# Performance work log

Measured on AMD Instinct MI355X. Metric: run time of the kernel, lower is better.

## Reference

```python
import jax, jax.numpy as jnp
import numpy as np

IN_F = 4096
OUT_F = 12288
GROUPSIZE = 128
BATCH = 8
N_GROUPS = IN_F // GROUPSIZE  # 32


def setup_inputs() -> dict:
    key = jax.random.key(0)
    k1, k2, k3, k4 = jax.random.split(key, 4)
    x = jax.random.normal(k1, (BATCH, IN_F), dtype=jnp.float32)
    # int4 codes in [0, 16)
    qweight = jax.random.randint(k2, (OUT_F, IN_F), 0, 16, dtype=jnp.int32)
    # per-group scales (positive, small) and zeros, layout [in//groupsize, out]
    scales = jax.random.uniform(k3, (N_GROUPS, OUT_F), dtype=jnp.float32) * 0.02 + 1e-3
    zeros = jax.random.normal(k4, (N_GROUPS, OUT_F), dtype=jnp.float32) * 0.1
    return {"x": x, "qweight": qweight, "scales": scales, "zeros": zeros}


def reference(x, qweight, scales, zeros):
    # Dequantize int4 weights: w = (q - 8) * scale + zero, per group of 128 along K.
    # qweight: [OUT_F, IN_F] -> [OUT_F, N_GROUPS, GROUPSIZE]
    q = qweight.reshape(OUT_F, N_GROUPS, GROUPSIZE).astype(jnp.float32)
    s = scales.T[:, :, None]  # [OUT_F, N_GROUPS, 1]
    z = zeros.T[:, :, None]   # [OUT_F, N_GROUPS, 1]
    w = ((q - 8.0) * s + z).reshape(OUT_F, IN_F)  # dequantized fp weight
    # Linear: y = x @ w.T  -> [BATCH, OUT_F]
    return jnp.einsum('bk,nk->bn', x, w)
```

## Files before the change

### kernel.cpp

```cpp
#include <hip/hip_runtime.h>

#define IN_F 4096
#define OUT_F 12288
#define BATCH 8
#define NGROUPS 32

#define CHUNK 256
#define NCHUNKS (IN_F / CHUNK)
#define ROWS_PER_WAVE 6
#define ROWS_PER_BLOCK 48
#define NBLOCKS (OUT_F / ROWS_PER_BLOCK)
#define THREADS 512

__global__ __launch_bounds__(THREADS, 2)
void w4a32_gemv(const float* __restrict__ x,
                const int* __restrict__ qw,
                const float* __restrict__ scales,
                const float* __restrict__ zeros,
                float* __restrict__ out)
{
    __shared__ float xs[BATCH][IN_F];
    __shared__ float szs[NGROUPS * ROWS_PER_BLOCK];
    __shared__ float szc[NGROUPS * ROWS_PER_BLOCK];

    const int tid   = threadIdx.x;
    const int wave  = tid >> 6;
    const int lane  = tid & 63;
    const int rowb  = blockIdx.x * ROWS_PER_BLOCK;
    const int wrow  = wave * ROWS_PER_WAVE;
    const int klane = lane << 2;

    const int* qbase = qw + (size_t)(rowb + wrow) * IN_F + klane;

    int4 qA[ROWS_PER_WAVE], qB[ROWS_PER_WAVE];
#pragma unroll
    for (int r = 0; r < ROWS_PER_WAVE; ++r)
        qA[r] = *reinterpret_cast<const int4*>(qbase + r * IN_F);

#pragma unroll
    for (int j = 0; j < 16; ++j) {
        const int idx = tid + j * THREADS;
        const int b   = idx >> 10;
        const int kk  = (idx & 1023) << 2;
        *reinterpret_cast<float4*>(&xs[b][kk]) =
            *reinterpret_cast<const float4*>(&x[b * IN_F + kk]);
    }
#pragma unroll
    for (int j = 0; j < 4; ++j) {
        const int idx = tid + j * THREADS;
        const int g   = idx >> 6;
        const int r   = idx & 63;
        if (r < ROWS_PER_BLOCK) {
            const float s = scales[g * OUT_F + rowb + r];
            const float z = zeros [g * OUT_F + rowb + r];
            szs[g * ROWS_PER_BLOCK + r] = s;
            szc[g * ROWS_PER_BLOCK + r] = __builtin_fmaf(s, -8.f, z);
        }
    }
    __syncthreads();

    float acc[ROWS_PER_WAVE][BATCH];
#pragma unroll
    for (int r = 0; r < ROWS_PER_WAVE; ++r)
#pragma unroll
        for (int b = 0; b < BATCH; ++b) acc[r][b] = 0.f;

    auto consume = [&](const int4 (&q)[ROWS_PER_WAVE], const int k0c) {
        const int g = (k0c >> 7) + (lane >> 5);
        float4 xr[BATCH];
#pragma unroll
        for (int b = 0; b < BATCH; ++b)
            xr[b] = *reinterpret_cast<const float4*>(&xs[b][k0c + klane]);
#pragma unroll
        for (int r = 0; r < ROWS_PER_WAVE; ++r) {
            const float s  = szs[g * ROWS_PER_BLOCK + wrow + r];
            const float cc = szc[g * ROWS_PER_BLOCK + wrow + r];
            const float w0 = __builtin_fmaf((float)q[r].x, s, cc);
            const float w1 = __builtin_fmaf((float)q[r].y, s, cc);
            const float w2 = __builtin_fmaf((float)q[r].z, s, cc);
            const float w3 = __builtin_fmaf((float)q[r].w, s, cc);
#pragma unroll
            for (int b = 0; b < BATCH; ++b) {
                float a = acc[r][b];
                a = __builtin_fmaf(w0, xr[b].x, a);
                a = __builtin_fmaf(w1, xr[b].y, a);
                a = __builtin_fmaf(w2, xr[b].z, a);
                a = __builtin_fmaf(w3, xr[b].w, a);
                acc[r][b] = a;
            }
        }
    };

    for (int c = 0; c < NCHUNKS; c += 2) {
        const int k0 = c * CHUNK;
#pragma unroll
        for (int r = 0; r < ROWS_PER_WAVE; ++r)
            qB[r] = *reinterpret_cast<const int4*>(qbase + r * IN_F + k0 + CHUNK);

        consume(qA, k0);

        if (c + 2 < NCHUNKS) {
#pragma unroll
            for (int r = 0; r < ROWS_PER_WAVE; ++r)
                qA[r] = *reinterpret_cast<const int4*>(qbase + r * IN_F + k0 + 2 * CHUNK);
        }

        consume(qB, k0 + CHUNK);
    }

#pragma unroll
    for (int r = 0; r < ROWS_PER_WAVE; ++r) {
        const int n = rowb + wrow + r;
#pragma unroll
        for (int b = 0; b < BATCH; ++b) {
            float v = acc[r][b];
            v += __shfl_xor(v, 32);
            v += __shfl_xor(v, 16);
            v += __shfl_xor(v, 8);
            v += __shfl_xor(v, 4);
            v += __shfl_xor(v, 2);
            v += __shfl_xor(v, 1);
            if (lane == b) out[b * OUT_F + n] = v;
        }
    }
}

extern "C" void kernel_launch(void* const* d_in, const int* in_sizes, int n_in,
                              void* d_out, int out_size, void* d_ws, size_t ws_size,
                              hipStream_t stream) {
    const float* x      = (const float*)d_in[0];
    const int*   qw     = (const int*)d_in[1];
    const float* scales = (const float*)d_in[2];
    const float* zeros  = (const float*)d_in[3];
    float* out = (float*)d_out;

    w4a32_gemv<<<NBLOCKS, THREADS, 0, stream>>>(x, qw, scales, zeros, out);
}
```

Baseline: 51.02 us.

## Double threads per block, halve rows per wave, use nontemporal weight loads

Measured after the change: 43.30 us. 15.1% less time.

```diff
diff --git a/kernel.cpp b/kernel.cpp
--- a/kernel.cpp
+++ b/kernel.cpp
@@ -5,14 +5,16 @@
 #define BATCH 8
 #define NGROUPS 32
 
+#define ROWS_PER_WAVE 3
+#define ROWS_PER_BLOCK 48
+#define NBLOCKS (OUT_F / ROWS_PER_BLOCK)
+#define THREADS 1024
 #define CHUNK 256
 #define NCHUNKS (IN_F / CHUNK)
-#define ROWS_PER_WAVE 6
-#define ROWS_PER_BLOCK 48
-#define NBLOCKS (OUT_F / ROWS_PER_BLOCK)
-#define THREADS 512
 
-__global__ __launch_bounds__(THREADS, 2)
+typedef int v4i __attribute__((ext_vector_type(4)));
+
+__global__ __launch_bounds__(THREADS, 4)
 void w4a32_gemv(const float* __restrict__ x,
                 const int* __restrict__ qw,
                 const float* __restrict__ scales,
@@ -30,15 +32,20 @@
     const int wrow  = wave * ROWS_PER_WAVE;
     const int klane = lane << 2;
 
-    const int* qbase = qw + (size_t)(rowb + wrow) * IN_F + klane;
+    const int* __restrict__ qbase = qw + (size_t)(rowb + wrow) * IN_F + klane;
 
-    int4 qA[ROWS_PER_WAVE], qB[ROWS_PER_WAVE];
-#pragma unroll
-    for (int r = 0; r < ROWS_PER_WAVE; ++r)
-        qA[r] = *reinterpret_cast<const int4*>(qbase + r * IN_F);
+#define ISSUE(B, c) do {                                                     \
+    _Pragma("unroll")                                                        \
+    for (int r = 0; r < ROWS_PER_WAVE; ++r)                                  \
+        B[r] = __builtin_nontemporal_load(                                   \
+            reinterpret_cast<const v4i*>(qbase + r * IN_F + (c) * CHUNK));   \
+    } while (0)
+
+    v4i qA[ROWS_PER_WAVE], qB[ROWS_PER_WAVE];
+    ISSUE(qA, 0);
 
 #pragma unroll
-    for (int j = 0; j < 16; ++j) {
+    for (int j = 0; j < 8; ++j) {
         const int idx = tid + j * THREADS;
         const int b   = idx >> 10;
         const int kk  = (idx & 1023) << 2;
@@ -46,7 +53,7 @@
             *reinterpret_cast<const float4*>(&x[b * IN_F + kk]);
     }
 #pragma unroll
-    for (int j = 0; j < 4; ++j) {
+    for (int j = 0; j < 2; ++j) {
         const int idx = tid + j * THREADS;
         const int g   = idx >> 6;
         const int r   = idx & 63;
@@ -65,48 +72,39 @@
 #pragma unroll
         for (int b = 0; b < BATCH; ++b) acc[r][b] = 0.f;
 
-    auto consume = [&](const int4 (&q)[ROWS_PER_WAVE], const int k0c) {
-        const int g = (k0c >> 7) + (lane >> 5);
-        float4 xr[BATCH];
-#pragma unroll
-        for (int b = 0; b < BATCH; ++b)
-            xr[b] = *reinterpret_cast<const float4*>(&xs[b][k0c + klane]);
-#pragma unroll
-        for (int r = 0; r < ROWS_PER_WAVE; ++r) {
-            const float s  = szs[g * ROWS_PER_BLOCK + wrow + r];
-            const float cc = szc[g * ROWS_PER_BLOCK + wrow + r];
-            const float w0 = __builtin_fmaf((float)q[r].x, s, cc);
-            const float w1 = __builtin_fmaf((float)q[r].y, s, cc);
-            const float w2 = __builtin_fmaf((float)q[r].z, s, cc);
-            const float w3 = __builtin_fmaf((float)q[r].w, s, cc);
-#pragma unroll
-            for (int b = 0; b < BATCH; ++b) {
-                float a = acc[r][b];
-                a = __builtin_fmaf(w0, xr[b].x, a);
-                a = __builtin_fmaf(w1, xr[b].y, a);
-                a = __builtin_fmaf(w2, xr[b].z, a);
-                a = __builtin_fmaf(w3, xr[b].w, a);
-                acc[r][b] = a;
-            }
-        }
-    };
+#define CONSUME(B, c) do {                                                   \
+    const int g = 2 * (c) + (lane >> 5);                                     \
+    float4 xr[BATCH];                                                        \
+    _Pragma("unroll")                                                        \
+    for (int b = 0; b < BATCH; ++b)                                          \
+        xr[b] = *reinterpret_cast<const float4*>(&xs[b][(c) * CHUNK + klane]);\
+    _Pragma("unroll")                                                        \
+    for (int r = 0; r < ROWS_PER_WAVE; ++r) {                                \
+        const float s  = szs[g * ROWS_PER_BLOCK + wrow + r];                 \
+        const float cc = szc[g * ROWS_PER_BLOCK + wrow + r];                 \
+        const float w0 = __builtin_fmaf((float)B[r][0], s, cc);              \
+        const float w1 = __builtin_fmaf((float)B[r][1], s, cc);              \
+        const float w2 = __builtin_fmaf((float)B[r][2], s, cc);              \
+        const float w3 = __builtin_fmaf((float)B[r][3], s, cc);              \
+        _Pragma("unroll")                                                    \
+        for (int b = 0; b < BATCH; ++b) {                                    \
+            float a = acc[r][b];                                             \
+            a = __builtin_fmaf(w0, xr[b].x, a);                              \
+            a = __builtin_fmaf(w1, xr[b].y, a);                              \
+            a = __builtin_fmaf(w2, xr[b].z, a);                              \
+            a = __builtin_fmaf(w3, xr[b].w, a);                              \
+            acc[r][b] = a;                                                   \
+        }                                                                    \
+    } } while (0)
 
     for (int c = 0; c < NCHUNKS; c += 2) {
-        const int k0 = c * CHUNK;
-#pragma unroll
-        for (int r = 0; r < ROWS_PER_WAVE; ++r)
-            qB[r] = *reinterpret_cast<const int4*>(qbase + r * IN_F + k0 + CHUNK);
-
-        consume(qA, k0);
-
-        if (c + 2 < NCHUNKS) {
-#pragma unroll
-            for (int r = 0; r < ROWS_PER_WAVE; ++r)
-                qA[r] = *reinterpret_cast<const int4*>(qbase + r * IN_F + k0 + 2 * CHUNK);
-        }
-
-        consume(qB, k0 + CHUNK);
+        ISSUE(qB, c + 1);
+        CONSUME(qA, c);
+        if (c + 2 < NCHUNKS) ISSUE(qA, c + 2);
+        CONSUME(qB, c + 1);
     }
+#undef ISSUE
+#undef CONSUME
 
 #pragma unroll
     for (int r = 0; r < ROWS_PER_WAVE; ++r) {
```
